# Kernel tuning notes

Hardware: AMD Instinct MI355X
Metric: run time of the kernel (lower is better)

The kernel has to match this reference:

```python
import jax, jax.numpy as jnp
import numpy as np

N_EMBD = 1024
N_HEAD = 16
HEAD = N_EMBD // N_HEAD


def setup_inputs() -> dict:
    key = jax.random.key(0)
    ks = jax.random.split(key, 6)
    B, S = 4, 2048
    scale = 1.0 / np.sqrt(N_EMBD)
    return {
        "x": jax.random.normal(ks[0], (B, S, N_EMBD), dtype=jnp.float32),
        "Wq": jax.random.normal(ks[1], (N_EMBD, N_EMBD), dtype=jnp.float32) * scale,
        "Wk": jax.random.normal(ks[2], (N_EMBD, N_EMBD), dtype=jnp.float32) * scale,
        "Wv": jax.random.normal(ks[3], (N_EMBD, N_EMBD), dtype=jnp.float32) * scale,
        "Wo": jax.random.normal(ks[4], (N_EMBD, N_EMBD), dtype=jnp.float32) * scale,
        "bo": jnp.zeros((N_EMBD,), dtype=jnp.float32),
    }


def reference(x, Wq, Wk, Wv, Wo, bo):
    B, S, _ = x.shape
    # projections; nn.Linear applies x @ W.T but W is random here, so x @ W is equivalent math
    def split_heads(t):  # (B,S,E) -> (B,H,S,D)
        return t.reshape(B, S, N_HEAD, HEAD).transpose(0, 2, 1, 3)

    q = split_heads(x @ Wq)
    k = split_heads(x @ Wk)
    v = split_heads(x @ Wv)
    scores = jnp.einsum("bhqd,bhkd->bhqk", q, k) * (HEAD ** -0.5)
    causal = jnp.tril(jnp.ones((S, S), dtype=bool))
    scores = jnp.where(causal, scores, -jnp.inf)
    weights = jax.nn.softmax(scores, axis=-1)  # dropout p=0 (eval)
    out = jnp.einsum("bhqk,bhkd->bhqd", weights, v)
    out = out.transpose(0, 2, 1, 3).reshape(B, S, N_EMBD)
    return out @ Wo + bo
```

## Files before the change

### kernel.cpp

```cpp
#include <hip/hip_runtime.h>
#include <hip/hip_bf16.h>

typedef unsigned short u16;
typedef unsigned int u32;
typedef __bf16 bf16x8 __attribute__((ext_vector_type(8)));
typedef float f32x4 __attribute__((ext_vector_type(4)));
typedef u16 u16x8 __attribute__((ext_vector_type(8)));
typedef u16 u16x4 __attribute__((ext_vector_type(4)));

#define NB 4
#define SEQ 2048
#define EMB 1024
#define NHEAD 16
#define DHEAD 64
#define MTOT (NB*SEQ)

static __device__ __forceinline__ u16 f2bf(float f) {
  union { __bf16 h; u16 u; } cv;
  cv.h = (__bf16)f;
  return cv.u;
}

static __device__ __forceinline__ float fexp2(float x) {
  float r;
  asm("v_exp_f32 %0, %1" : "=v"(r) : "v"(x));
  return r;
}

static __device__ __forceinline__ void gload16(const void* g, void* l) {
  __builtin_amdgcn_global_load_lds((const __attribute__((address_space(1))) void*)g,
                                   (__attribute__((address_space(3))) void*)l, 16, 0, 0);
}


__global__ __launch_bounds__(256) void k_cvt_x(const float* __restrict__ in, u16* __restrict__ out) {
  size_t i = (size_t)blockIdx.x * 256 + threadIdx.x;
  const float4* p = (const float4*)in + i * 2;
  float4 a = p[0], b = p[1];
  u16x8 r;
  r[0] = f2bf(a.x); r[1] = f2bf(a.y); r[2] = f2bf(a.z); r[3] = f2bf(a.w);
  r[4] = f2bf(b.x); r[5] = f2bf(b.y); r[6] = f2bf(b.z); r[7] = f2bf(b.w);
  *(u16x8*)(out + i * 8) = r;
}

__global__ __launch_bounds__(256) void k_wtrans(const float* __restrict__ W0, const float* __restrict__ W1,
                                                const float* __restrict__ W2, const float* __restrict__ W3,
                                                u16* __restrict__ O0, u16* __restrict__ O1,
                                                u16* __restrict__ O2, u16* __restrict__ O3) {
  __shared__ float tile[64][65];
  const float* W = blockIdx.z == 0 ? W0 : blockIdx.z == 1 ? W1 : blockIdx.z == 2 ? W2 : W3;
  u16* O       = blockIdx.z == 0 ? O0 : blockIdx.z == 1 ? O1 : blockIdx.z == 2 ? O2 : O3;
  const int c0 = blockIdx.x * 64, r0 = blockIdx.y * 64;
  const int t = threadIdx.x;
  const int tr = t >> 4, tc = (t & 15) * 4;
#pragma unroll
  for (int p = 0; p < 4; p++) {
    int r = tr + p * 16;
    float4 v = *(const float4*)&W[(size_t)(r0 + r) * EMB + c0 + tc];
    tile[r][tc + 0] = v.x; tile[r][tc + 1] = v.y; tile[r][tc + 2] = v.z; tile[r][tc + 3] = v.w;
  }
  __syncthreads();
#pragma unroll
  for (int p = 0; p < 4; p++) {
    int orow = tr + p * 16;
    u16x4 o;
    o[0] = f2bf(tile[tc + 0][orow]); o[1] = f2bf(tile[tc + 1][orow]);
    o[2] = f2bf(tile[tc + 2][orow]); o[3] = f2bf(tile[tc + 3][orow]);
    *(u16x4*)&O[(size_t)(c0 + orow) * EMB + r0 + tc] = o;
  }
}


static __device__ __forceinline__ void gemm_core(const u16* __restrict__ A, const u16* __restrict__ BT,
                                                 int m0, int n0, f32x4 acc[4][4]) {
  __shared__ u16 As[2][128 * 64];
  __shared__ u16 Bs[2][128 * 64];
  const int t = threadIdx.x, l = t & 63, w = t >> 6;
  const int g = l >> 4, q = l & 15;
  const int wm = (w >> 1) * 64, wn = (w & 1) * 64;

  const f32x4 zero4 = {0.f, 0.f, 0.f, 0.f};
#pragma unroll
  for (int mi = 0; mi < 4; mi++)
#pragma unroll
    for (int ni = 0; ni < 4; ni++) acc[mi][ni] = zero4;

  int srow[4], skel[4];
#pragma unroll
  for (int i = 0; i < 4; i++) {
    int row = w * 32 + i * 8 + (l >> 3);
    srow[i] = row; skel[i] = ((l & 7) ^ (row & 7)) * 8;
  }

  auto stage = [&](int k0, int bsel) {
    char* AsB = (char*)As[bsel] + w * 4096;
    char* BsB = (char*)Bs[bsel] + w * 4096;
#pragma unroll
    for (int i = 0; i < 4; i++) {
      gload16(A + (size_t)(m0 + srow[i]) * EMB + k0 + skel[i], AsB + i * 1024);
      gload16(BT + (size_t)(n0 + srow[i]) * EMB + k0 + skel[i], BsB + i * 1024);
    }
  };

  auto compute = [&](int bsel) {
    char* AsB = (char*)As[bsel];
    char* BsB = (char*)Bs[bsel];
#pragma unroll
    for (int kc = 0; kc < 2; kc++) {
      bf16x8 af[4], bfv[4];
#pragma unroll
      for (int mi = 0; mi < 4; mi++) {
        int row = wm + mi * 16 + q;
        af[mi] = *(const bf16x8*)(AsB + row * 128 + (((kc * 4 + g) ^ (row & 7)) << 4));
      }
#pragma unroll
      for (int ni = 0; ni < 4; ni++) {
        int row = wn + ni * 16 + q;
        bfv[ni] = *(const bf16x8*)(BsB + row * 128 + (((kc * 4 + g) ^ (row & 7)) << 4));
      }
      __builtin_amdgcn_s_setprio(1);
#pragma unroll
      for (int mi = 0; mi < 4; mi++)
#pragma unroll
        for (int ni = 0; ni < 4; ni++)
          acc[mi][ni] = __builtin_amdgcn_mfma_f32_16x16x32_bf16(af[mi], bfv[ni], acc[mi][ni], 0, 0, 0);
      __builtin_amdgcn_s_setprio(0);
    }
  };

  stage(0, 0);
  int buf = 0;
  for (int k0 = 64; k0 <= EMB; k0 += 64) {
    const bool pf = (k0 < EMB);
    if (pf) {
      stage(k0, buf ^ 1);
      asm volatile("s_waitcnt vmcnt(8)" ::: "memory");
    } else {
      asm volatile("s_waitcnt vmcnt(0)" ::: "memory");
    }
    __builtin_amdgcn_s_barrier();
    __builtin_amdgcn_sched_barrier(0);
    compute(buf);
    asm volatile("s_waitcnt lgkmcnt(0)" ::: "memory");
    __builtin_amdgcn_s_barrier();
    buf ^= 1;
  }
}

__global__ __launch_bounds__(256) void k_gemm_qkv(const u16* __restrict__ xb, const u16* __restrict__ Wqkv,
                                                  u16* __restrict__ Qb, u16* __restrict__ Kb, u16* __restrict__ Vb) {
  const int wg = blockIdx.x;
  const int c = wg & 7, local = wg >> 3;
  const int mi_ = local & 63, ni_ = c * 3 + (local >> 6);
  const int m0 = mi_ * 128, n0 = ni_ * 128;

  f32x4 acc[4][4];
  gemm_core(xb, Wqkv, m0, n0, acc);

  const int z = n0 >> 10;
  u16* Out = z == 0 ? Qb : (z == 1 ? Kb : Vb);
  const float scale = z == 0 ? 0.125f * 1.4426950408889634f : 1.0f;

  const int t = threadIdx.x, l = t & 63, w = t >> 6;
  const int g = l >> 4, q = l & 15;
  const int wm = (w >> 1) * 64, wn = (w & 1) * 64;
#pragma unroll
  for (int mi = 0; mi < 4; mi++)
#pragma unroll
    for (int ni = 0; ni < 4; ni++)
#pragma unroll
      for (int jj = 0; jj < 4; jj++) {
        int m = m0 + wm + mi * 16 + g * 4 + jj;
        int n = n0 + wn + ni * 16 + q;
        int b = m >> 11, s = m & 2047;
        int col = n & 1023;
        int h = col >> 6, d = col & 63;
        Out[(((size_t)(b * NHEAD + h)) * SEQ + s) * DHEAD + d] = f2bf(acc[mi][ni][jj] * scale);
      }
}

__global__ __launch_bounds__(256) void k_gemm_out(const u16* __restrict__ Ob, const u16* __restrict__ WoT,
                                                  const float* __restrict__ bo, float* __restrict__ out) {
  const int wg = blockIdx.x;
  const int c = wg & 7, local = wg >> 3;
  const int m0 = (local & 63) * 128, n0 = c * 128;

  f32x4 acc[4][4];
  gemm_core(Ob, WoT, m0, n0, acc);

  const int t = threadIdx.x, l = t & 63, w = t >> 6;
  const int g = l >> 4, q = l & 15;
  const int wm = (w >> 1) * 64, wn = (w & 1) * 64;
#pragma unroll
  for (int ni = 0; ni < 4; ni++) {
    int n = n0 + wn + ni * 16 + q;
    float bv = bo[n];
#pragma unroll
    for (int mi = 0; mi < 4; mi++)
#pragma unroll
      for (int jj = 0; jj < 4; jj++) {
        int m = m0 + wm + mi * 16 + g * 4 + jj;
        out[(size_t)m * EMB + n] = acc[mi][ni][jj] + bv;
      }
  }
}

__global__ __launch_bounds__(256, 4) void k_attn(const u16* __restrict__ Qb, const u16* __restrict__ Kb,
                                                 const u16* __restrict__ Vb, u16* __restrict__ Ob) {
  __shared__ u16 Ks[2][64 * 64];
  __shared__ u16 Vt[2][64 * 64];
  const int t = threadIdx.x, l = t & 63, w = t >> 6;
  const int g = l >> 4, q = l & 15;
  const int bh = blockIdx.x;
  const int b = bh >> 4, h = bh & 15;
  const size_t hb = (size_t)bh * SEQ * DHEAD;
  const float NEG_INF = -__builtin_inff();

  const int i = blockIdx.y;
  const int qA0 = i * 64, qB0 = (31 - i) * 64;
  const int ntA = i + 1, ntB = 32 - i;

  int krow[2], kel[2];
#pragma unroll
  for (int ii = 0; ii < 2; ii++) {
    int row = w * 16 + ii * 8 + (l >> 3);
    krow[ii] = row; kel[ii] = ((l & 7) ^ (row & 7)) * 8;
  }
  const int kp = t & 31, d0v = (t >> 5) * 8;
  const int r2 = 2 * kp;
  const int sp = 32 * ((r2 >> 4) >> 1) + 8 * ((r2 >> 2) & 3) + 4 * ((r2 >> 4) & 1) + (r2 & 3);

  auto stageK = [&](int kbase, int bsel) {
    char* dst = (char*)Ks[bsel] + w * 2048;
#pragma unroll
    for (int ii = 0; ii < 2; ii++)
      gload16(Kb + hb + (size_t)(kbase + krow[ii]) * DHEAD + kel[ii], dst + ii * 1024);
  };
  auto loadV = [&](int kbase, u16x8& v0, u16x8& v1) {
    v0 = *(const u16x8*)(Vb + hb + (size_t)(kbase + 2 * kp) * DHEAD + d0v);
    v1 = *(const u16x8*)(Vb + hb + (size_t)(kbase + 2 * kp + 1) * DHEAD + d0v);
  };
  auto writeV = [&](int bsel, const u16x8& v0, const u16x8& v1) {
    char* VtB = (char*)Vt[bsel];
#pragma unroll
    for (int ii = 0; ii < 8; ii++) {
      int d = d0v + ii;
      u32 val = (u32)v0[ii] | ((u32)v1[ii] << 16);
      *(u32*)(VtB + d * 128 + ((sp * 2) ^ ((d & 7) << 4))) = val;
    }
  };

  bf16x8 qfA[2], qfB[2];
#pragma unroll
  for (int kc = 0; kc < 2; kc++) {
    qfA[kc] = *(const bf16x8*)(Qb + hb + (size_t)(qA0 + w * 16 + q) * DHEAD + kc * 32 + g * 8);
    qfB[kc] = *(const bf16x8*)(Qb + hb + (size_t)(qB0 + w * 16 + q) * DHEAD + kc * 32 + g * 8);
  }
  const int qglobA = qA0 + w * 16 + q, qglobB = qB0 + w * 16 + q;

  f32x4 oA[4], oB[4];
  const f32x4 zero4 = {0.f, 0.f, 0.f, 0.f};
#pragma unroll
  for (int df = 0; df < 4; df++) { oA[df] = zero4; oB[df] = zero4; }
  float mA = NEG_INF, lA = 0.f, mB = NEG_INF, lB = 0.f;

  auto compute = [&](const bf16x8 (&qf)[2], f32x4 (&o)[4], float& m_run, float& l_run,
                     bool diag, int qglob, int k0, char* KsB, char* VtB) {
    f32x4 st[4];
#pragma unroll
    for (int kf = 0; kf < 4; kf++) st[kf] = zero4;
    __builtin_amdgcn_s_setprio(1);
#pragma unroll
    for (int kc = 0; kc < 2; kc++)
#pragma unroll
      for (int kf = 0; kf < 4; kf++) {
        int key = kf * 16 + q;
        bf16x8 a = *(const bf16x8*)(KsB + key * 128 + (((kc * 4 + g) ^ (key & 7)) << 4));
        st[kf] = __builtin_amdgcn_mfma_f32_16x16x32_bf16(a, qf[kc], st[kf], 0, 0, 0);
      }
    __builtin_amdgcn_s_setprio(0);

    if (diag) {
#pragma unroll
      for (int kf = 0; kf < 4; kf++)
#pragma unroll
        for (int jj = 0; jj < 4; jj++)
          if (k0 + kf * 16 + g * 4 + jj > qglob) st[kf][jj] = NEG_INF;
    }

    f32x4 mv;
#pragma unroll
    for (int jj = 0; jj < 4; jj++)
      mv[jj] = fmaxf(fmaxf(st[0][jj], st[1][jj]), fmaxf(st[2][jj], st[3][jj]));
    float smax = fmaxf(fmaxf(mv[0], mv[1]), fmaxf(mv[2], mv[3]));
    smax = fmaxf(smax, __shfl_xor(smax, 16));
    smax = fmaxf(smax, __shfl_xor(smax, 32));

    if (!__all(smax - m_run <= 8.0f)) {
      float mnew = fmaxf(m_run, smax);
      float sc = fexp2(m_run - mnew);
      l_run *= sc;
#pragma unroll
      for (int jj = 0; jj < 4; jj++) {
        float scj = __shfl(sc, g * 4 + jj);
#pragma unroll
        for (int df = 0; df < 4; df++) o[df][jj] *= scj;
      }
      m_run = mnew;
    }

    f32x4 pv[4];
#pragma unroll
    for (int kf = 0; kf < 4; kf++)
#pragma unroll
      for (int jj = 0; jj < 4; jj++)
        pv[kf][jj] = fexp2(st[kf][jj] - m_run);
    f32x4 sv = (pv[0] + pv[1]) + (pv[2] + pv[3]);
    float psum = (sv[0] + sv[1]) + (sv[2] + sv[3]);
    psum += __shfl_xor(psum, 16);
    psum += __shfl_xor(psum, 32);
    l_run += psum;

    bf16x8 pa[2];
    pa[0] = bf16x8{ (__bf16)pv[0][0], (__bf16)pv[0][1], (__bf16)pv[0][2], (__bf16)pv[0][3],
                    (__bf16)pv[1][0], (__bf16)pv[1][1], (__bf16)pv[1][2], (__bf16)pv[1][3] };
    pa[1] = bf16x8{ (__bf16)pv[2][0], (__bf16)pv[2][1], (__bf16)pv[2][2], (__bf16)pv[2][3],
                    (__bf16)pv[3][0], (__bf16)pv[3][1], (__bf16)pv[3][2], (__bf16)pv[3][3] };

    __builtin_amdgcn_s_setprio(1);
#pragma unroll
    for (int kc = 0; kc < 2; kc++) {
#pragma unroll
      for (int df = 0; df < 4; df++) {
        int d = df * 16 + q;
        bf16x8 vb = *(const bf16x8*)(VtB + d * 128 + (((kc * 4 + g) ^ (d & 7)) << 4));
        o[df] = __builtin_amdgcn_mfma_f32_16x16x32_bf16(pa[kc], vb, o[df], 0, 0, 0);
      }
    }
    __builtin_amdgcn_s_setprio(0);
  };

  {
    u16x8 v0, v1;
    stageK(0, 0);
    loadV(0, v0, v1);
    writeV(0, v0, v1);
  }
  __syncthreads();

  int buf = 0;
  for (int kt = 0; kt < ntB; ++kt) {
    const int k0 = kt * 64;
    const bool pf = (kt + 1 < ntB);
    u16x8 nv0, nv1;
    if (pf) {
      stageK((kt + 1) * 64, buf ^ 1);
      loadV((kt + 1) * 64, nv0, nv1);
    }
    char* KsB = (char*)Ks[buf];
    char* VtB = (char*)Vt[buf];

    compute(qfB, oB, mB, lB, kt == ntB - 1, qglobB, k0, KsB, VtB);
    __builtin_amdgcn_sched_barrier(0);
    if (kt < ntA)
      compute(qfA, oA, mA, lA, kt == ntA - 1, qglobA, k0, KsB, VtB);

    if (pf) writeV(buf ^ 1, nv0, nv1);
    __syncthreads();
    buf ^= 1;
  }

  auto store = [&](f32x4 (&o)[4], float l_run, int q0) {
    float inv = 1.f / l_run;
#pragma unroll
    for (int jj = 0; jj < 4; jj++) {
      float r = __shfl(inv, g * 4 + jj);
      int s = q0 + w * 16 + g * 4 + jj;
#pragma unroll
      for (int df = 0; df < 4; df++)
        Ob[((size_t)(b * SEQ + s)) * EMB + h * DHEAD + df * 16 + q] = f2bf(o[df][jj] * r);
    }
  };
  store(oA, lA, qA0);
  store(oB, lB, qB0);
}


extern "C" void kernel_launch(void* const* d_in, const int* in_sizes, int n_in,
                              void* d_out, int out_size, void* d_ws, size_t ws_size,
                              hipStream_t stream) {
  const float* x  = (const float*)d_in[0];
  const float* Wq = (const float*)d_in[1];
  const float* Wk = (const float*)d_in[2];
  const float* Wv = (const float*)d_in[3];
  const float* Wo = (const float*)d_in[4];
  const float* bo = (const float*)d_in[5];
  float* out = (float*)d_out;

  char* ws = (char*)d_ws;
  u16* xb  = (u16*)(ws);
  u16* WqT = (u16*)(ws + (16u << 20));
  u16* WkT = WqT + (size_t)EMB * EMB;
  u16* WvT = WkT + (size_t)EMB * EMB;
  u16* WoT = WvT + (size_t)EMB * EMB;
  u16* Qb  = (u16*)(ws + (24u << 20));
  u16* Kb  = Qb + (size_t)MTOT * EMB;
  u16* Vb  = Kb + (size_t)MTOT * EMB;
  u16* Ob  = Vb + (size_t)MTOT * EMB;

  k_cvt_x<<<dim3(4096), 256, 0, stream>>>(x, xb);
  k_wtrans<<<dim3(16, 16, 4), 256, 0, stream>>>(Wq, Wk, Wv, Wo, WqT, WkT, WvT, WoT);
  k_gemm_qkv<<<dim3(1536), 256, 0, stream>>>(xb, WqT, Qb, Kb, Vb);
  k_attn<<<dim3(64, 16), 256, 0, stream>>>(Qb, Kb, Vb, Ob);
  k_gemm_out<<<dim3(512), 256, 0, stream>>>(Ob, WoT, bo, out);
}
```

Before: 171.7 us.

## Enlarge QKV GEMM tiles to 256x256 with 512-thread workgroups

```diff
diff --git a/kernel.cpp b/kernel.cpp
--- a/kernel.cpp
+++ b/kernel.cpp
@@ -147,25 +147,95 @@
   }
 }
 
-__global__ __launch_bounds__(256) void k_gemm_qkv(const u16* __restrict__ xb, const u16* __restrict__ Wqkv,
-                                                  u16* __restrict__ Qb, u16* __restrict__ Kb, u16* __restrict__ Vb) {
+__global__ __launch_bounds__(512, 2) void k_gemm_qkv(const u16* __restrict__ xb, const u16* __restrict__ Wqkv,
+                                                     u16* __restrict__ Qb, u16* __restrict__ Kb, u16* __restrict__ Vb) {
+  __shared__ u16 As[2][256 * 64];
+  __shared__ u16 Bs[2][256 * 64];
+  const int t = threadIdx.x, l = t & 63, wid = t >> 6;
+  const int g = l >> 4, q = l & 15;
+  const int wr = wid >> 2, wc = wid & 3;
+  const int wm = wr * 128, wn = wc * 64;
+
   const int wg = blockIdx.x;
   const int c = wg & 7, local = wg >> 3;
-  const int mi_ = local & 63, ni_ = c * 3 + (local >> 6);
-  const int m0 = mi_ * 128, n0 = ni_ * 128;
-
-  f32x4 acc[4][4];
-  gemm_core(xb, Wqkv, m0, n0, acc);
+  const int idx = c * 48 + local;
+  const int ni_ = idx >> 5, mi_ = idx & 31;
+  const int m0 = mi_ * 256, n0 = ni_ * 256;
+
+  f32x4 acc[8][4];
+  const f32x4 zero4 = {0.f, 0.f, 0.f, 0.f};
+#pragma unroll
+  for (int mi = 0; mi < 8; mi++)
+#pragma unroll
+    for (int ni = 0; ni < 4; ni++) acc[mi][ni] = zero4;
+
+  int srow[4], skel[4];
+#pragma unroll
+  for (int i = 0; i < 4; i++) {
+    int row = i * 64 + (t >> 3);
+    srow[i] = row; skel[i] = ((t & 7) ^ (row & 7)) * 8;
+  }
+
+  auto stage = [&](int k0, int bsel) {
+    char* Ab = (char*)As[bsel] + wid * 1024;
+    char* Bb = (char*)Bs[bsel] + wid * 1024;
+#pragma unroll
+    for (int i = 0; i < 4; i++) {
+      gload16(xb   + (size_t)(m0 + srow[i]) * EMB + k0 + skel[i], Ab + i * 8192);
+      gload16(Wqkv + (size_t)(n0 + srow[i]) * EMB + k0 + skel[i], Bb + i * 8192);
+    }
+  };
+
+  auto compute = [&](int bsel) {
+    char* Ab = (char*)As[bsel];
+    char* Bb = (char*)Bs[bsel];
+#pragma unroll
+    for (int kc = 0; kc < 2; kc++) {
+      bf16x8 af[8], bfv[4];
+#pragma unroll
+      for (int mi = 0; mi < 8; mi++) {
+        int row = wm + mi * 16 + q;
+        af[mi] = *(const bf16x8*)(Ab + row * 128 + (((kc * 4 + g) ^ (row & 7)) << 4));
+      }
+#pragma unroll
+      for (int ni = 0; ni < 4; ni++) {
+        int row = wn + ni * 16 + q;
+        bfv[ni] = *(const bf16x8*)(Bb + row * 128 + (((kc * 4 + g) ^ (row & 7)) << 4));
+      }
+      __builtin_amdgcn_s_setprio(1);
+#pragma unroll
+      for (int mi = 0; mi < 8; mi++)
+#pragma unroll
+        for (int ni = 0; ni < 4; ni++)
+          acc[mi][ni] = __builtin_amdgcn_mfma_f32_16x16x32_bf16(af[mi], bfv[ni], acc[mi][ni], 0, 0, 0);
+      __builtin_amdgcn_s_setprio(0);
+    }
+  };
+
+  stage(0, 0);
+  int buf = 0;
+  for (int k0 = 64; k0 <= EMB; k0 += 64) {
+    const bool pf = (k0 < EMB);
+    if (pf) {
+      stage(k0, buf ^ 1);
+      asm volatile("s_waitcnt vmcnt(8)" ::: "memory");
+    } else {
+      asm volatile("s_waitcnt vmcnt(0)" ::: "memory");
+    }
+    __builtin_amdgcn_s_barrier();
+    __builtin_amdgcn_sched_barrier(0);
+    compute(buf);
+    asm volatile("s_waitcnt lgkmcnt(0)" ::: "memory");
+    __builtin_amdgcn_s_barrier();
+    buf ^= 1;
+  }
 
   const int z = n0 >> 10;
   u16* Out = z == 0 ? Qb : (z == 1 ? Kb : Vb);
   const float scale = z == 0 ? 0.125f * 1.4426950408889634f : 1.0f;
 
-  const int t = threadIdx.x, l = t & 63, w = t >> 6;
-  const int g = l >> 4, q = l & 15;
-  const int wm = (w >> 1) * 64, wn = (w & 1) * 64;
-#pragma unroll
-  for (int mi = 0; mi < 4; mi++)
+#pragma unroll
+  for (int mi = 0; mi < 8; mi++)
 #pragma unroll
     for (int ni = 0; ni < 4; ni++)
 #pragma unroll
@@ -410,7 +480,7 @@
 
   k_cvt_x<<<dim3(4096), 256, 0, stream>>>(x, xb);
   k_wtrans<<<dim3(16, 16, 4), 256, 0, stream>>>(Wq, Wk, Wv, Wo, WqT, WkT, WvT, WoT);
-  k_gemm_qkv<<<dim3(1536), 256, 0, stream>>>(xb, WqT, Qb, Kb, Vb);
+  k_gemm_qkv<<<dim3(384), 512, 0, stream>>>(xb, WqT, Qb, Kb, Vb);
   k_attn<<<dim3(64, 16), 256, 0, stream>>>(Qb, Kb, Vb, Ob);
   k_gemm_out<<<dim3(512), 256, 0, stream>>>(Ob, WoT, bo, out);
 }
```

New measurement: 173.9 us. Within noise of the previous version (+1.3%).

## Rewrite QKV GEMM with 256x256 tiles, 8 waves, and interleaved quarter-tile pipeline

Applied to the files above, without the earlier changes.

```diff
diff --git a/kernel.cpp b/kernel.cpp
--- a/kernel.cpp
+++ b/kernel.cpp
@@ -147,36 +147,141 @@
   }
 }
 
-__global__ __launch_bounds__(256) void k_gemm_qkv(const u16* __restrict__ xb, const u16* __restrict__ Wqkv,
-                                                  u16* __restrict__ Qb, u16* __restrict__ Kb, u16* __restrict__ Vb) {
+__global__ __launch_bounds__(512, 2) void k_gemm_qkv(const u16* __restrict__ xb, const u16* __restrict__ Wqkv,
+                                                     u16* __restrict__ Qb, u16* __restrict__ Kb, u16* __restrict__ Vb) {
+  __shared__ u16 As[2][256 * 64];
+  __shared__ u16 Bs[2][256 * 64];
+  const int t = threadIdx.x, l = t & 63, wid = t >> 6;
+  const int g = l >> 4, q = l & 15;
+  const int wr = wid >> 2, wc = wid & 3;
+
   const int wg = blockIdx.x;
   const int c = wg & 7, local = wg >> 3;
-  const int mi_ = local & 63, ni_ = c * 3 + (local >> 6);
-  const int m0 = mi_ * 128, n0 = ni_ * 128;
-
-  f32x4 acc[4][4];
-  gemm_core(xb, Wqkv, m0, n0, acc);
+  const int idx = c * 48 + local;
+  const int ni_ = idx >> 5, mi_ = idx & 31;
+  const int m0 = mi_ * 256, n0 = ni_ * 256;
+
+  f32x4 acc[2][2][4][2];
+  const f32x4 zero4 = {0.f, 0.f, 0.f, 0.f};
+#pragma unroll
+  for (int R = 0; R < 2; R++)
+#pragma unroll
+    for (int C = 0; C < 2; C++)
+#pragma unroll
+      for (int mi = 0; mi < 4; mi++)
+#pragma unroll
+        for (int ni = 0; ni < 2; ni++) acc[R][C][mi][ni] = zero4;
+
+  int srow[2], skel[2];
+#pragma unroll
+  for (int j = 0; j < 2; j++) {
+    int row = j * 64 + (t >> 3);
+    srow[j] = row; skel[j] = ((t & 7) ^ (row & 7)) * 8;
+  }
+
+  auto stageHalf = [&](int op, int half, int tile) {
+    if (tile >= 16) return;
+    const int kk = tile * 64, d = tile & 1;
+    const u16* src = op ? Wqkv : xb;
+    const int base = op ? n0 : m0;
+    char* dst = (char*)(op ? Bs[d] : As[d]) + half * 16384 + wid * 1024;
+#pragma unroll
+    for (int j = 0; j < 2; j++)
+      gload16(src + (size_t)(base + half * 128 + srow[j]) * EMB + kk + skel[j], dst + j * 8192);
+  };
+
+  bf16x8 af[4][2], bf0[2][2], bf1[2][2];
+  auto loadA = [&](int R, int d) {
+    char* Ab = (char*)As[d];
+#pragma unroll
+    for (int mi = 0; mi < 4; mi++)
+#pragma unroll
+      for (int kc = 0; kc < 2; kc++) {
+        int row = R * 128 + wr * 64 + mi * 16 + q;
+        af[mi][kc] = *(const bf16x8*)(Ab + row * 128 + (((kc * 4 + g) ^ (row & 7)) << 4));
+      }
+  };
+  auto loadB = [&](int C, int d, bf16x8 (&bfv)[2][2]) {
+    char* Bb = (char*)Bs[d];
+#pragma unroll
+    for (int ni = 0; ni < 2; ni++)
+#pragma unroll
+      for (int kc = 0; kc < 2; kc++) {
+        int row = C * 128 + wc * 32 + ni * 16 + q;
+        bfv[ni][kc] = *(const bf16x8*)(Bb + row * 128 + (((kc * 4 + g) ^ (row & 7)) << 4));
+      }
+  };
+
+#define MFMA16(R, C, BF)                                                                   \
+  do {                                                                                     \
+    __builtin_amdgcn_s_setprio(1);                                                         \
+    _Pragma("unroll")                                                                      \
+    for (int kc = 0; kc < 2; kc++)                                                         \
+      _Pragma("unroll")                                                                    \
+      for (int mi = 0; mi < 4; mi++)                                                       \
+        _Pragma("unroll")                                                                  \
+        for (int ni = 0; ni < 2; ni++)                                                     \
+          acc[R][C][mi][ni] = __builtin_amdgcn_mfma_f32_16x16x32_bf16(af[mi][kc], BF[ni][kc], acc[R][C][mi][ni], 0, 0, 0); \
+    __builtin_amdgcn_s_setprio(0);                                                         \
+  } while (0)
+
+  stageHalf(0, 0, 0); stageHalf(1, 0, 0); stageHalf(1, 1, 0); stageHalf(0, 1, 0);
+  stageHalf(0, 0, 1); stageHalf(1, 1, 1);
+  asm volatile("s_waitcnt vmcnt(4)" ::: "memory");
+  __builtin_amdgcn_s_barrier();
+  __builtin_amdgcn_sched_barrier(0);
+
+  for (int kt = 0; kt < 16; ++kt) {
+    const int d = kt & 1;
+    loadA(0, d); loadB(0, d, bf0);
+    stageHalf(0, 1, kt + 1);
+    __builtin_amdgcn_s_barrier();
+    MFMA16(0, 0, bf0);
+    __builtin_amdgcn_s_barrier();
+    __builtin_amdgcn_sched_barrier(0);
+    loadB(1, d, bf1);
+    stageHalf(1, 0, kt + 1);
+    __builtin_amdgcn_s_barrier();
+    MFMA16(0, 1, bf1);
+    __builtin_amdgcn_s_barrier();
+    __builtin_amdgcn_sched_barrier(0);
+    loadA(1, d);
+    stageHalf(0, 0, kt + 2);
+    __builtin_amdgcn_s_barrier();
+    MFMA16(1, 1, bf1);
+    __builtin_amdgcn_s_barrier();
+    __builtin_amdgcn_sched_barrier(0);
+    stageHalf(1, 1, kt + 2);
+    __builtin_amdgcn_s_barrier();
+    MFMA16(1, 0, bf0);
+    if (kt <= 13)      asm volatile("s_waitcnt vmcnt(4)" ::: "memory");
+    else if (kt == 14) asm volatile("s_waitcnt vmcnt(0)" ::: "memory");
+    __builtin_amdgcn_s_barrier();
+    __builtin_amdgcn_sched_barrier(0);
+  }
+#undef MFMA16
 
   const int z = n0 >> 10;
   u16* Out = z == 0 ? Qb : (z == 1 ? Kb : Vb);
   const float scale = z == 0 ? 0.125f * 1.4426950408889634f : 1.0f;
 
-  const int t = threadIdx.x, l = t & 63, w = t >> 6;
-  const int g = l >> 4, q = l & 15;
-  const int wm = (w >> 1) * 64, wn = (w & 1) * 64;
-#pragma unroll
-  for (int mi = 0; mi < 4; mi++)
-#pragma unroll
-    for (int ni = 0; ni < 4; ni++)
-#pragma unroll
-      for (int jj = 0; jj < 4; jj++) {
-        int m = m0 + wm + mi * 16 + g * 4 + jj;
-        int n = n0 + wn + ni * 16 + q;
-        int b = m >> 11, s = m & 2047;
-        int col = n & 1023;
-        int h = col >> 6, d = col & 63;
-        Out[(((size_t)(b * NHEAD + h)) * SEQ + s) * DHEAD + d] = f2bf(acc[mi][ni][jj] * scale);
-      }
+#pragma unroll
+  for (int R = 0; R < 2; R++)
+#pragma unroll
+    for (int C = 0; C < 2; C++)
+#pragma unroll
+      for (int mi = 0; mi < 4; mi++)
+#pragma unroll
+        for (int ni = 0; ni < 2; ni++)
+#pragma unroll
+          for (int jj = 0; jj < 4; jj++) {
+            int m = m0 + R * 128 + wr * 64 + mi * 16 + g * 4 + jj;
+            int n = n0 + C * 128 + wc * 32 + ni * 16 + q;
+            int b = m >> 11, s = m & 2047;
+            int col = n & 1023;
+            int h = col >> 6, dd = col & 63;
+            Out[(((size_t)(b * NHEAD + h)) * SEQ + s) * DHEAD + dd] = f2bf(acc[R][C][mi][ni][jj] * scale);
+          }
 }
 
 __global__ __launch_bounds__(256) void k_gemm_out(const u16* __restrict__ Ob, const u16* __restrict__ WoT,
@@ -410,7 +515,7 @@
 
   k_cvt_x<<<dim3(4096), 256, 0, stream>>>(x, xb);
   k_wtrans<<<dim3(16, 16, 4), 256, 0, stream>>>(Wq, Wk, Wv, Wo, WqT, WkT, WvT, WoT);
-  k_gemm_qkv<<<dim3(1536), 256, 0, stream>>>(xb, WqT, Qb, Kb, Vb);
+  k_gemm_qkv<<<dim3(384), 512, 0, stream>>>(xb, WqT, Qb, Kb, Vb);
   k_attn<<<dim3(64, 16), 256, 0, stream>>>(Qb, Kb, Vb, Ob);
   k_gemm_out<<<dim3(512), 256, 0, stream>>>(Ob, WoT, bo, out);
 }
```

Result: faster. 166.5 us (-3.0%).
